# Optimization experiments

Measured on AMD Instinct MI355X. Metric: run time of the kernel, lower is better.

## Reference

```python
import jax, jax.numpy as jnp
import numpy as np

DIM = 1024
N_HEADS = 16
HEAD_DIM = DIM // N_HEADS
B, T = 2, 2048


def setup_inputs() -> dict:
    key = jax.random.key(0)
    ks = jax.random.split(key, 5)
    s = 0.02
    return {
        "x": jax.random.normal(ks[0], (B, T, DIM), dtype=jnp.float32),
        "w_qkv": jax.random.normal(ks[1], (DIM, 3 * DIM), dtype=jnp.float32) * s,
        "b_qkv": jnp.zeros((3 * DIM,), dtype=jnp.float32),
        "w_proj": jax.random.normal(ks[2], (DIM, DIM), dtype=jnp.float32) * s,
        "b_proj": jnp.zeros((DIM,), dtype=jnp.float32),
    }


def reference(x, w_qkv, b_qkv, w_proj, b_proj):
    Bb, Tt, C = x.shape
    H, Dh = N_HEADS, HEAD_DIM
    qkv = x @ w_qkv + b_qkv                       # [B,T,3C]
    qkv = qkv.reshape(Bb, Tt, 3, H, Dh)
    q = jnp.transpose(qkv[:, :, 0], (0, 2, 1, 3))  # [B,H,T,Dh]
    k = jnp.transpose(qkv[:, :, 1], (0, 2, 1, 3))
    v = jnp.transpose(qkv[:, :, 2], (0, 2, 1, 3))
    att = jnp.einsum("bhqd,bhkd->bhqk", q, k) / jnp.sqrt(jnp.float32(Dh))
    causal = jnp.tril(jnp.ones((Tt, Tt), dtype=bool))
    att = jnp.where(causal[None, None], att, -jnp.inf)
    att = jax.nn.softmax(att, axis=-1)
    out = jnp.einsum("bhqk,bhkd->bhqd", att, v)    # [B,H,T,Dh]
    out = jnp.transpose(out, (0, 2, 1, 3)).reshape(Bb, Tt, C)
    return out @ w_proj + b_proj
```

## Files before the change

### kernel.cpp

```cpp
#include <hip/hip_runtime.h>
#include <math.h>

#define DIMC 1024
#define NH 16
#define HD 64
#define BATCH 2
#define SEQ 2048
#define M_ROWS (BATCH * SEQ)
#define QKV_N (3 * DIMC)

typedef __attribute__((ext_vector_type(8))) short bf16x8;
typedef __attribute__((ext_vector_type(4))) float f32x4;
typedef __attribute__((ext_vector_type(2))) unsigned int u32x2;

static __device__ __forceinline__ unsigned short f2bf(float f) {
    union { float f; unsigned u; } v; v.f = f;
    unsigned r = v.u + 0x7fffu + ((v.u >> 16) & 1u);
    return (unsigned short)(r >> 16);
}

static __device__ __forceinline__ unsigned cvt_pk_bf16(float lo, float hi) {
    unsigned r;
    asm("v_cvt_pk_bf16_f32 %0, %1, %2" : "=v"(r) : "v"(lo), "v"(hi));
    return r;
}

#define GLOAD16(g, l)                                                          \
    __builtin_amdgcn_global_load_lds(                                          \
        (__attribute__((address_space(1))) void*)(void*)(g),                   \
        (__attribute__((address_space(3))) void*)(void*)(l), 16, 0, 0)

__global__ __launch_bounds__(256) void cvt_bf16(const float* __restrict__ in,
                                                short* __restrict__ out)
{
    int i = blockIdx.x * 256 + threadIdx.x;
    float4 v = reinterpret_cast<const float4*>(in)[i];
    ushort4 o = {f2bf(v.x), f2bf(v.y), f2bf(v.z), f2bf(v.w)};
    reinterpret_cast<ushort4*>(out)[i] = o;
}

__global__ __launch_bounds__(256) void transpose_bf16(const float* __restrict__ in,
                                                      short* __restrict__ out,
                                                      int R, int C)
{
    __shared__ short tile[64][65];
    const int tid = threadIdx.x;
    const int r0 = blockIdx.y * 64, c0 = blockIdx.x * 64;
    #pragma unroll
    for (int i = 0; i < 4; ++i) {
        int r = i * 16 + (tid >> 4);
        int c = (tid & 15) * 4;
        float4 v = *reinterpret_cast<const float4*>(&in[(size_t)(r0 + r) * C + c0 + c]);
        tile[c + 0][r] = f2bf(v.x);
        tile[c + 1][r] = f2bf(v.y);
        tile[c + 2][r] = f2bf(v.z);
        tile[c + 3][r] = f2bf(v.w);
    }
    __syncthreads();
    #pragma unroll
    for (int i = 0; i < 4; ++i) {
        int c = i * 16 + (tid >> 4);
        int r = (tid & 15) * 4;
        ushort4 o;
        o.x = tile[c][r + 0]; o.y = tile[c][r + 1];
        o.z = tile[c][r + 2]; o.w = tile[c][r + 3];
        *reinterpret_cast<ushort4*>(&out[(size_t)(c0 + c) * R + r0 + r]) = o;
    }
}

template<int EPI>
__global__ __launch_bounds__(256) void gemm_mfma(const short* __restrict__ A,
                                                 const short* __restrict__ Bt,
                                                 const float* __restrict__ bias,
                                                 float* __restrict__ C,
                                                 short* __restrict__ Qb,
                                                 short* __restrict__ Kb,
                                                 short* __restrict__ Vt,
                                                 int M, int N, int K)
{
    __shared__ short As[128 * 32];
    __shared__ short Bs[128 * 32];

    const int tid  = threadIdx.x;
    const int wave = tid >> 6;
    const int lane = tid & 63;
    const int l16  = lane & 15;
    const int lg   = lane >> 4;
    const int wr   = wave >> 1;
    const int wc   = wave & 1;

    const int brow = blockIdx.y * 128;
    const int bcol = blockIdx.x * 128;

    const int srow   = tid >> 2;
    const int schunk = (tid & 3) * 8;
    const short* ga0 = A  + (size_t)(brow + srow) * K + schunk;
    const short* gb0 = Bt + (size_t)(bcol + srow) * K + schunk;

    f32x4 acc[4][4] = {};

    for (int k0 = 0; k0 < K; k0 += 32) {
        __syncthreads();
        GLOAD16(ga0 + k0,          &As[tid * 8]);
        GLOAD16(ga0 + 64 * K + k0, &As[2048 + tid * 8]);
        GLOAD16(gb0 + k0,          &Bs[tid * 8]);
        GLOAD16(gb0 + 64 * K + k0, &Bs[2048 + tid * 8]);
        __syncthreads();

        bf16x8 af[4], bf[4];
        #pragma unroll
        for (int m = 0; m < 4; ++m)
            af[m] = *reinterpret_cast<const bf16x8*>(
                &As[(wr * 64 + m * 16 + l16) * 32 + lg * 8]);
        #pragma unroll
        for (int n = 0; n < 4; ++n)
            bf[n] = *reinterpret_cast<const bf16x8*>(
                &Bs[(wc * 64 + n * 16 + l16) * 32 + lg * 8]);
        #pragma unroll
        for (int m = 0; m < 4; ++m)
            #pragma unroll
            for (int n = 0; n < 4; ++n)
                acc[m][n] = __builtin_amdgcn_mfma_f32_16x16x32_bf16(
                    af[m], bf[n], acc[m][n], 0, 0, 0);
    }

    if (EPI == 0) {
        #pragma unroll
        for (int m = 0; m < 4; ++m) {
            #pragma unroll
            for (int n = 0; n < 4; ++n) {
                int col = bcol + wc * 64 + n * 16 + l16;
                float bv = bias[col];
                #pragma unroll
                for (int r = 0; r < 4; ++r) {
                    int row = brow + wr * 64 + m * 16 + lg * 4 + r;
                    C[(size_t)row * N + col] = acc[m][n][r] + bv;
                }
            }
        }
    } else {
        const int sec = bcol >> 10;
        #pragma unroll
        for (int m = 0; m < 4; ++m) {
            const int t0 = brow + wr * 64 + m * 16 + lg * 4;
            const int bb = t0 >> 11;
            const int tl = t0 & 2047;
            #pragma unroll
            for (int n = 0; n < 4; ++n) {
                int col = bcol + wc * 64 + n * 16 + l16;
                int hh  = (col & 1023) >> 6;
                int d   = col & 63;
                float bv = bias[col];
                if (sec == 0) {
                    #pragma unroll
                    for (int r = 0; r < 4; ++r)
                        Qb[((size_t)(bb * NH + hh) * SEQ + tl + r) * HD + d] =
                            (short)f2bf((acc[m][n][r] + bv) * 0.18033688011112042f);
                } else if (sec == 1) {
                    #pragma unroll
                    for (int r = 0; r < 4; ++r)
                        Kb[((size_t)(bb * NH + hh) * SEQ + tl + r) * HD + d] =
                            (short)f2bf(acc[m][n][r] + bv);
                } else {
                    ushort4 o;
                    o.x = f2bf(acc[m][n][0] + bv);
                    o.y = f2bf(acc[m][n][1] + bv);
                    o.z = f2bf(acc[m][n][2] + bv);
                    o.w = f2bf(acc[m][n][3] + bv);
                    *reinterpret_cast<ushort4*>(
                        &Vt[((size_t)(bb * NH + hh) * HD + d) * SEQ + tl]) = o;
                }
            }
        }
    }
}

static __device__ __forceinline__ void attn_step_sw(const bf16x8 qf[2],
                                                    f32x4 acc[4],
                                                    float& lsum,
                                                    const char* kshc, const char* vshc,
                                                    char* pw,
                                                    int l16, int lg,
                                                    bool do_mask, int qloc)
{
    const f32x4 fzero = {0.f, 0.f, 0.f, 0.f};
    f32x4 sa[4];
    __builtin_amdgcn_s_setprio(1);
    #pragma unroll
    for (int kc = 0; kc < 4; ++kc) {
        sa[kc] = fzero;
        int row = kc * 16 + l16;
        #pragma unroll
        for (int c = 0; c < 2; ++c) {
            int byte = (row << 7) + (c << 6) + (lg << 4);
            byte ^= ((row & 7) << 4);
            bf16x8 kf = *reinterpret_cast<const bf16x8*>(kshc + byte);
            sa[kc] = __builtin_amdgcn_mfma_f32_16x16x32_bf16(kf, qf[c], sa[kc], 0, 0, 0);
        }
    }
    __builtin_amdgcn_s_setprio(0);

    #pragma unroll
    for (int kc = 0; kc < 4; ++kc) {
        const int kl = kc * 16 + lg * 4;
        float p0, p1, p2, p3;
        {
            float s0 = sa[kc][0], s1 = sa[kc][1], s2 = sa[kc][2], s3 = sa[kc][3];
            if (do_mask) {
                if (kl + 0 > qloc) s0 = -1e30f;
                if (kl + 1 > qloc) s1 = -1e30f;
                if (kl + 2 > qloc) s2 = -1e30f;
                if (kl + 3 > qloc) s3 = -1e30f;
            }
            p0 = exp2f(s0); p1 = exp2f(s1); p2 = exp2f(s2); p3 = exp2f(s3);
        }
        lsum += (p0 + p1) + (p2 + p3);
        u32x2 pk;
        pk.x = cvt_pk_bf16(p0, p1);
        pk.y = cvt_pk_bf16(p2, p3);
        int byte = (l16 << 7) + (kc << 5) + (lg << 3);
        byte ^= ((l16 & 7) << 4);
        *reinterpret_cast<u32x2*>(pw + byte) = pk;
    }

    __builtin_amdgcn_s_setprio(1);
    #pragma unroll
    for (int c = 0; c < 2; ++c) {
        int pbyte = (l16 << 7) + (c << 6) + (lg << 4);
        pbyte ^= ((l16 & 7) << 4);
        bf16x8 pf = *reinterpret_cast<const bf16x8*>(pw + pbyte);
        #pragma unroll
        for (int dg = 0; dg < 4; ++dg) {
            int vrow  = dg * 16 + l16;
            int vbyte = (vrow << 7) + (c << 6) + (lg << 4);
            vbyte ^= ((vrow & 7) << 4);
            bf16x8 vf = *reinterpret_cast<const bf16x8*>(vshc + vbyte);
            acc[dg] = __builtin_amdgcn_mfma_f32_16x16x32_bf16(pf, vf, acc[dg], 0, 0, 0);
        }
    }
    __builtin_amdgcn_s_setprio(0);
}

__global__ __launch_bounds__(256, 2) void attn_mfma(const short* __restrict__ Qb,
                                                    const short* __restrict__ Kb,
                                                    const short* __restrict__ Vt,
                                                    short* __restrict__ out)
{
    const int tid  = threadIdx.x;
    const int wave = tid >> 6;
    const int lane = tid & 63;
    const int l16  = lane & 15;
    const int lg   = lane >> 4;

    const int raw = blockIdx.x;
    const int wg  = (raw & 7) * 64 + (raw >> 3);
    const int i = wg & 15;
    const int h = (wg >> 4) & 15;
    const int b = wg >> 8;

    const int wp  = wave >> 1;
    const int wro = (wave & 1) * 16;
    const int qtA = 2 * i + wp;
    const int qtB = 63 - 2 * i - wp;
    const int ktA = i;
    const int ktB = 31 - i;

    __shared__ short ksh[64 * 64];
    __shared__ short vsh[64 * 64];
    __shared__ short psh[4][16 * 64];

    const short* qgb = Qb + (size_t)(b * NH + h) * SEQ * HD;
    bf16x8 qfA[2], qfB[2];
    {
        const short* qa = qgb + (size_t)(qtA * 32 + wro + l16) * HD;
        qfA[0] = *reinterpret_cast<const bf16x8*>(qa + 8 * lg);
        qfA[1] = *reinterpret_cast<const bf16x8*>(qa + 32 + 8 * lg);
        const short* qb = qgb + (size_t)(qtB * 32 + wro + l16) * HD;
        qfB[0] = *reinterpret_cast<const bf16x8*>(qb + 8 * lg);
        qfB[1] = *reinterpret_cast<const bf16x8*>(qb + 32 + 8 * lg);
    }

    const short* kgb = Kb + (size_t)(b * NH + h) * SEQ * HD;
    const short* vgb = Vt + (size_t)(b * NH + h) * HD * SEQ;

    const int row0 = tid >> 3;
    const int col0 = (tid & 7) * 8;

    bf16x8 kreg[2], vreg[2];
    #pragma unroll
    for (int it = 0; it < 2; ++it) {
        int row = row0 + it * 32;
        kreg[it] = *reinterpret_cast<const bf16x8*>(kgb + (size_t)row * HD + col0);
        vreg[it] = *reinterpret_cast<const bf16x8*>(vgb + (size_t)row * SEQ + col0);
    }

    f32x4 accA[4] = {}, accB[4] = {};
    float lsumA = 0.f, lsumB = 0.f;

    const int qlocA = (qtA & 1) * 32 + wro + l16;
    const int qlocB = (qtB & 1) * 32 + wro + l16;
    char* pw = (char*)psh[wave];

    for (int kt = 0; kt <= ktB; ++kt) {
        __syncthreads();
        #pragma unroll
        for (int it = 0; it < 2; ++it) {
            int row  = row0 + it * 32;
            int byte = (row << 7) + (col0 << 1);
            byte ^= ((row & 7) << 4);
            *reinterpret_cast<bf16x8*>((char*)ksh + byte) = kreg[it];
            *reinterpret_cast<bf16x8*>((char*)vsh + byte) = vreg[it];
        }
        if (kt < ktB) {
            #pragma unroll
            for (int it = 0; it < 2; ++it) {
                int row = row0 + it * 32;
                kreg[it] = *reinterpret_cast<const bf16x8*>(
                    kgb + (size_t)((kt + 1) * 64 + row) * HD + col0);
                vreg[it] = *reinterpret_cast<const bf16x8*>(
                    vgb + (size_t)row * SEQ + (kt + 1) * 64 + col0);
            }
        }
        __syncthreads();

        attn_step_sw(qfB, accB, lsumB, (const char*)ksh, (const char*)vsh, pw,
                     l16, lg, kt == ktB, qlocB);
        if (kt <= ktA)
            attn_step_sw(qfA, accA, lsumA, (const char*)ksh, (const char*)vsh, pw,
                         l16, lg, kt == ktA, qlocA);
    }

    lsumA += __shfl_xor(lsumA, 16);
    lsumA += __shfl_xor(lsumA, 32);
    lsumB += __shfl_xor(lsumB, 16);
    lsumB += __shfl_xor(lsumB, 32);
    const float linvA = 1.0f / lsumA;
    const float linvB = 1.0f / lsumB;

    #pragma unroll
    for (int r = 0; r < 4; ++r) {
        float invA = __shfl(linvA, lg * 4 + r);
        float invB = __shfl(linvB, lg * 4 + r);
        int qa = qtA * 32 + wro + lg * 4 + r;
        int qb = qtB * 32 + wro + lg * 4 + r;
        short* opa = out + ((size_t)(b * SEQ + qa)) * DIMC + h * HD;
        short* opb = out + ((size_t)(b * SEQ + qb)) * DIMC + h * HD;
        #pragma unroll
        for (int dg = 0; dg < 4; ++dg) {
            opa[dg * 16 + l16] = (short)f2bf(accA[dg][r] * invA);
            opb[dg * 16 + l16] = (short)f2bf(accB[dg][r] * invB);
        }
    }
}

extern "C" void kernel_launch(void* const* d_in, const int* in_sizes, int n_in,
                              void* d_out, int out_size, void* d_ws, size_t ws_size,
                              hipStream_t stream)
{
    const float* x      = (const float*)d_in[0];
    const float* w_qkv  = (const float*)d_in[1];
    const float* b_qkv  = (const float*)d_in[2];
    const float* w_proj = (const float*)d_in[3];
    const float* b_proj = (const float*)d_in[4];
    float* out = (float*)d_out;

    short* Qb   = (short*)d_ws;
    short* Kb   = Qb + (size_t)M_ROWS * DIMC;
    short* Vt   = Kb + (size_t)M_ROWS * DIMC;
    short* attn = Vt + (size_t)M_ROWS * DIMC;
    short* xb   = attn + (size_t)M_ROWS * DIMC;
    short* Wqt  = xb + (size_t)M_ROWS * DIMC;
    short* Wpt  = Wqt + (size_t)DIMC * QKV_N;

    cvt_bf16<<<dim3(M_ROWS * DIMC / 4 / 256), dim3(256), 0, stream>>>(x, xb);
    transpose_bf16<<<dim3(QKV_N / 64, DIMC / 64), dim3(256), 0, stream>>>(
        w_qkv, Wqt, DIMC, QKV_N);
    transpose_bf16<<<dim3(DIMC / 64, DIMC / 64), dim3(256), 0, stream>>>(
        w_proj, Wpt, DIMC, DIMC);

    gemm_mfma<1><<<dim3(QKV_N / 128, M_ROWS / 128), dim3(256), 0, stream>>>(
        xb, Wqt, b_qkv, nullptr, Qb, Kb, Vt, M_ROWS, QKV_N, DIMC);

    attn_mfma<<<dim3(BATCH * NH * 16), dim3(256), 0, stream>>>(Qb, Kb, Vt, attn);

    gemm_mfma<0><<<dim3(DIMC / 128, M_ROWS / 128), dim3(256), 0, stream>>>(
        attn, Wpt, b_proj, out, nullptr, nullptr, nullptr, M_ROWS, DIMC, DIMC);
}
```

Measured before the change: 123.0 us.

## Merge weight transposes, deepen GEMM K-step, remap blocks, split attention into smaller workgroups

Fuses the two weight transpose launches into a single kernel. The GEMM now loads a 64-wide K slab per iteration, which halves the number of barriers, and it remaps block indices so that row tiles group together for L2 locality. Attention goes from 512 blocks of 256 threads to 1024 blocks of 128 threads, each block handling one balanced query-tile pair, for better load balance and occupancy. The GEMM remap hardcodes 32 row tiles (by = nf & 31). That matches M_ROWS/128 = 32, but it ties the kernel to this shape.

```diff
diff --git a/kernel.cpp b/kernel.cpp
--- a/kernel.cpp
+++ b/kernel.cpp
@@ -39,13 +39,20 @@
     reinterpret_cast<ushort4*>(out)[i] = o;
 }
 
-__global__ __launch_bounds__(256) void transpose_bf16(const float* __restrict__ in,
-                                                      short* __restrict__ out,
-                                                      int R, int C)
+__global__ __launch_bounds__(256) void transpose_both(const float* __restrict__ wq,
+                                                      short* __restrict__ wqt,
+                                                      const float* __restrict__ wp,
+                                                      short* __restrict__ wpt)
 {
     __shared__ short tile[64][65];
     const int tid = threadIdx.x;
-    const int r0 = blockIdx.y * 64, c0 = blockIdx.x * 64;
+    const bool isq = blockIdx.x < 48;
+    const int bx  = isq ? blockIdx.x : blockIdx.x - 48;
+    const int C   = isq ? QKV_N : DIMC;
+    const float* in = isq ? wq : wp;
+    short* out      = isq ? wqt : wpt;
+    const int R = DIMC;
+    const int r0 = blockIdx.y * 64, c0 = bx * 64;
     #pragma unroll
     for (int i = 0; i < 4; ++i) {
         int r = i * 16 + (tid >> 4);
@@ -78,8 +85,8 @@
                                                  short* __restrict__ Vt,
                                                  int M, int N, int K)
 {
-    __shared__ short As[128 * 32];
-    __shared__ short Bs[128 * 32];
+    __shared__ short As[2][128 * 32];
+    __shared__ short Bs[2][128 * 32];
 
     const int tid  = threadIdx.x;
     const int wave = tid >> 6;
@@ -89,39 +96,54 @@
     const int wr   = wave >> 1;
     const int wc   = wave & 1;
 
-    const int brow = blockIdx.y * 128;
-    const int bcol = blockIdx.x * 128;
-
-    const int srow   = tid >> 2;
-    const int schunk = (tid & 3) * 8;
-    const short* ga0 = A  + (size_t)(brow + srow) * K + schunk;
-    const short* gb0 = Bt + (size_t)(bcol + srow) * K + schunk;
+    const int nx   = gridDim.x;
+    const int flat = blockIdx.y * nx + blockIdx.x;
+    const int nwg  = nx * gridDim.y;
+    const int q8   = nwg >> 3;
+    const int nf   = (flat & 7) * q8 + (flat >> 3);
+    const int by   = nf & 31;
+    const int bx   = nf >> 5;
+
+    const int brow = by * 128;
+    const int bcol = bx * 128;
+
+    const short* ga = A  + (size_t)brow * K;
+    const short* gb = Bt + (size_t)bcol * K;
 
     f32x4 acc[4][4] = {};
 
-    for (int k0 = 0; k0 < K; k0 += 32) {
+    for (int k0 = 0; k0 < K; k0 += 64) {
         __syncthreads();
-        GLOAD16(ga0 + k0,          &As[tid * 8]);
-        GLOAD16(ga0 + 64 * K + k0, &As[2048 + tid * 8]);
-        GLOAD16(gb0 + k0,          &Bs[tid * 8]);
-        GLOAD16(gb0 + 64 * K + k0, &Bs[2048 + tid * 8]);
+        #pragma unroll
+        for (int li = 0; li < 4; ++li) {
+            int c   = li * 256 + tid;
+            int ks  = c >> 9;
+            int row = (c & 511) >> 2;
+            int sub = c & 3;
+            size_t goff = (size_t)row * K + k0 + ks * 32 + sub * 8;
+            GLOAD16(ga + goff, &As[0][0] + c * 8);
+            GLOAD16(gb + goff, &Bs[0][0] + c * 8);
+        }
         __syncthreads();
 
-        bf16x8 af[4], bf[4];
-        #pragma unroll
-        for (int m = 0; m < 4; ++m)
-            af[m] = *reinterpret_cast<const bf16x8*>(
-                &As[(wr * 64 + m * 16 + l16) * 32 + lg * 8]);
-        #pragma unroll
-        for (int n = 0; n < 4; ++n)
-            bf[n] = *reinterpret_cast<const bf16x8*>(
-                &Bs[(wc * 64 + n * 16 + l16) * 32 + lg * 8]);
-        #pragma unroll
-        for (int m = 0; m < 4; ++m)
+        #pragma unroll
+        for (int ks = 0; ks < 2; ++ks) {
+            bf16x8 af[4], bf[4];
+            #pragma unroll
+            for (int m = 0; m < 4; ++m)
+                af[m] = *reinterpret_cast<const bf16x8*>(
+                    &As[ks][(wr * 64 + m * 16 + l16) * 32 + lg * 8]);
             #pragma unroll
             for (int n = 0; n < 4; ++n)
-                acc[m][n] = __builtin_amdgcn_mfma_f32_16x16x32_bf16(
-                    af[m], bf[n], acc[m][n], 0, 0, 0);
+                bf[n] = *reinterpret_cast<const bf16x8*>(
+                    &Bs[ks][(wc * 64 + n * 16 + l16) * 32 + lg * 8]);
+            #pragma unroll
+            for (int m = 0; m < 4; ++m)
+                #pragma unroll
+                for (int n = 0; n < 4; ++n)
+                    acc[m][n] = __builtin_amdgcn_mfma_f32_16x16x32_bf16(
+                        af[m], bf[n], acc[m][n], 0, 0, 0);
+        }
     }
 
     if (EPI == 0) {
@@ -241,10 +263,10 @@
     __builtin_amdgcn_s_setprio(0);
 }
 
-__global__ __launch_bounds__(256, 2) void attn_mfma(const short* __restrict__ Qb,
-                                                    const short* __restrict__ Kb,
-                                                    const short* __restrict__ Vt,
-                                                    short* __restrict__ out)
+__global__ __launch_bounds__(128) void attn_mfma(const short* __restrict__ Qb,
+                                                 const short* __restrict__ Kb,
+                                                 const short* __restrict__ Vt,
+                                                 short* __restrict__ out)
 {
     const int tid  = threadIdx.x;
     const int wave = tid >> 6;
@@ -253,21 +275,20 @@
     const int lg   = lane >> 4;
 
     const int raw = blockIdx.x;
-    const int wg  = (raw & 7) * 64 + (raw >> 3);
-    const int i = wg & 15;
-    const int h = (wg >> 4) & 15;
-    const int b = wg >> 8;
-
-    const int wp  = wave >> 1;
-    const int wro = (wave & 1) * 16;
-    const int qtA = 2 * i + wp;
-    const int qtB = 63 - 2 * i - wp;
-    const int ktA = i;
-    const int ktB = 31 - i;
+    const int wg  = (raw & 7) * 128 + (raw >> 3);
+    const int i = wg & 31;
+    const int h = (wg >> 5) & 15;
+    const int b = wg >> 9;
+
+    const int qtA = i;
+    const int qtB = 63 - i;
+    const int ktA = i >> 1;
+    const int ktB = (63 - i) >> 1;
+    const int wro = wave * 16;
 
     __shared__ short ksh[64 * 64];
     __shared__ short vsh[64 * 64];
-    __shared__ short psh[4][16 * 64];
+    __shared__ short psh[2][16 * 64];
 
     const short* qgb = Qb + (size_t)(b * NH + h) * SEQ * HD;
     bf16x8 qfA[2], qfB[2];
@@ -286,10 +307,10 @@
     const int row0 = tid >> 3;
     const int col0 = (tid & 7) * 8;
 
-    bf16x8 kreg[2], vreg[2];
-    #pragma unroll
-    for (int it = 0; it < 2; ++it) {
-        int row = row0 + it * 32;
+    bf16x8 kreg[4], vreg[4];
+    #pragma unroll
+    for (int it = 0; it < 4; ++it) {
+        int row = row0 + it * 16;
         kreg[it] = *reinterpret_cast<const bf16x8*>(kgb + (size_t)row * HD + col0);
         vreg[it] = *reinterpret_cast<const bf16x8*>(vgb + (size_t)row * SEQ + col0);
     }
@@ -300,12 +321,14 @@
     const int qlocA = (qtA & 1) * 32 + wro + l16;
     const int qlocB = (qtB & 1) * 32 + wro + l16;
     char* pw = (char*)psh[wave];
+    const char* kshc = (const char*)ksh;
+    const char* vshc = (const char*)vsh;
 
     for (int kt = 0; kt <= ktB; ++kt) {
         __syncthreads();
         #pragma unroll
-        for (int it = 0; it < 2; ++it) {
-            int row  = row0 + it * 32;
+        for (int it = 0; it < 4; ++it) {
+            int row  = row0 + it * 16;
             int byte = (row << 7) + (col0 << 1);
             byte ^= ((row & 7) << 4);
             *reinterpret_cast<bf16x8*>((char*)ksh + byte) = kreg[it];
@@ -313,8 +336,8 @@
         }
         if (kt < ktB) {
             #pragma unroll
-            for (int it = 0; it < 2; ++it) {
-                int row = row0 + it * 32;
+            for (int it = 0; it < 4; ++it) {
+                int row = row0 + it * 16;
                 kreg[it] = *reinterpret_cast<const bf16x8*>(
                     kgb + (size_t)((kt + 1) * 64 + row) * HD + col0);
                 vreg[it] = *reinterpret_cast<const bf16x8*>(
@@ -323,10 +346,10 @@
         }
         __syncthreads();
 
-        attn_step_sw(qfB, accB, lsumB, (const char*)ksh, (const char*)vsh, pw,
+        attn_step_sw(qfB, accB, lsumB, kshc, vshc, pw,
                      l16, lg, kt == ktB, qlocB);
         if (kt <= ktA)
-            attn_step_sw(qfA, accA, lsumA, (const char*)ksh, (const char*)vsh, pw,
+            attn_step_sw(qfA, accA, lsumA, kshc, vshc, pw,
                          l16, lg, kt == ktA, qlocA);
     }
 
@@ -373,15 +396,12 @@
     short* Wpt  = Wqt + (size_t)DIMC * QKV_N;
 
     cvt_bf16<<<dim3(M_ROWS * DIMC / 4 / 256), dim3(256), 0, stream>>>(x, xb);
-    transpose_bf16<<<dim3(QKV_N / 64, DIMC / 64), dim3(256), 0, stream>>>(
-        w_qkv, Wqt, DIMC, QKV_N);
-    transpose_bf16<<<dim3(DIMC / 64, DIMC / 64), dim3(256), 0, stream>>>(
-        w_proj, Wpt, DIMC, DIMC);
+    transpose_both<<<dim3(64, 16), dim3(256), 0, stream>>>(w_qkv, Wqt, w_proj, Wpt);
 
     gemm_mfma<1><<<dim3(QKV_N / 128, M_ROWS / 128), dim3(256), 0, stream>>>(
         xb, Wqt, b_qkv, nullptr, Qb, Kb, Vt, M_ROWS, QKV_N, DIMC);
 
-    attn_mfma<<<dim3(BATCH * NH * 16), dim3(256), 0, stream>>>(Qb, Kb, Vt, attn);
+    attn_mfma<<<dim3(BATCH * NH * 32), dim3(128), 0, stream>>>(Qb, Kb, Vt, attn);
 
     gemm_mfma<0><<<dim3(DIMC / 128, M_ROWS / 128), dim3(256), 0, stream>>>(
         attn, Wpt, b_proj, out, nullptr, nullptr, nullptr, M_ROWS, DIMC, DIMC);
```

After: 118.8 us. 3.4% less time.
